# Kernel tuning notes

Hardware: AMD Instinct MI355X
Metric: run time of the kernel (lower is better)

The kernel has to match this reference:

```python
import jax, jax.numpy as jnp
import numpy as np

# Model constants (match init_kwargs)
IN_DIM = 1024   # input_dim == OLA frame size
ST_DIM = 128    # state_dim
HOP = IN_DIM // 2
N_FRAMES = 512
N_SAMPLES = 262144  # n_frames * hop
CTX = 512       # context_dim == control_plane_dim
HD = 32         # hypernetwork_dim
HL = 16         # hypernetwork_latent
B = 8


def _make_w(hv, A, Bm, i, o):
    # HyperNetworkLayer: hypervector -> latent -> flattened (i, o) matrix per batch
    return (hv @ A @ Bm).reshape(-1, i, o)


def setup_inputs() -> dict:
    key = jax.random.key(0)
    ks = jax.random.split(key, 17)
    s = 0.05
    return {
        'control_signal': jax.random.normal(ks[0], (B, CTX, N_FRAMES), jnp.float32),
        'state_hv': jax.random.normal(ks[1], (B, HD), jnp.float32),
        'output_hv': jax.random.normal(ks[2], (B, HD), jnp.float32),
        'input_hv': jax.random.normal(ks[3], (B, HD), jnp.float32),
        'direct_hv': jax.random.normal(ks[4], (B, HD), jnp.float32),
        'proj_hv': jax.random.normal(ks[5], (B, HD), jnp.float32),
        'times': jax.random.normal(ks[6], (B, 1, N_FRAMES), jnp.float32),
        # hypernetwork parameters (learned)
        'A_proj': jax.random.normal(ks[7], (HD, HL), jnp.float32) * s,
        'B_proj': jax.random.normal(ks[8], (HL, CTX * IN_DIM), jnp.float32) * s,
        'A_state': jax.random.normal(ks[9], (HD, HL), jnp.float32) * s,
        'B_state': jax.random.normal(ks[10], (HL, ST_DIM * ST_DIM), jnp.float32) * s,
        'A_input': jax.random.normal(ks[11], (HD, HL), jnp.float32) * s,
        'B_input': jax.random.normal(ks[12], (HL, IN_DIM * ST_DIM), jnp.float32) * s,
        'A_output': jax.random.normal(ks[13], (HD, HL), jnp.float32) * s,
        'B_output': jax.random.normal(ks[14], (HL, ST_DIM * IN_DIM), jnp.float32) * s,
        'A_direct': jax.random.normal(ks[15], (HD, HL), jnp.float32) * s,
        'B_direct': jax.random.normal(ks[16], (HL, IN_DIM * IN_DIM), jnp.float32) * s,
    }


def _forward(control_signal, state_hv, output_hv, input_hv, direct_hv, proj_hv, times,
             A_proj, B_proj, A_state, B_state, A_input, B_input,
             A_output, B_output, A_direct, B_direct):
    batch = control_signal.shape[0]
    dt = control_signal.dtype
    # per-batch hypernetwork-generated dense matrices
    Wp = _make_w(proj_hv, A_proj, B_proj, CTX, IN_DIM)       # [b, ctx, in]
    Ws = _make_w(state_hv, A_state, B_state, ST_DIM, ST_DIM)  # [b, st, st]
    Wi = _make_w(input_hv, A_input, B_input, IN_DIM, ST_DIM)  # [b, in, st]
    Wo = _make_w(output_hv, A_output, B_output, ST_DIM, IN_DIM)
    Wd = _make_w(direct_hv, A_direct, B_direct, IN_DIM, IN_DIM)

    ctrl = jnp.transpose(control_signal ** 2, (0, 2, 1))       # [b, fr, ctx]
    proj = jnp.einsum('bfc,bci->bfi', ctrl, Wp)                # [b, fr, in]

    def step(s, u):
        # s_i = A s_{i-1} + B u_i ; y_i = C (A s_{i-1}) + D u_i
        s2 = jnp.einsum('bs,bst->bt', s, Ws)
        y = jnp.einsum('bt,bti->bi', s2, Wo) + jnp.einsum('bi,bij->bj', u, Wd)
        s_new = s2 + jnp.einsum('bi,bis->bs', u, Wi)
        return s_new, y

    s0 = jnp.zeros((batch, ST_DIM), dt)
    _, outs = jax.lax.scan(step, s0, jnp.transpose(proj, (1, 0, 2)))  # [fr, b, in]
    outs = jnp.transpose(outs, (1, 0, 2))                              # [b, fr, in]

    # overlap-add with periodic hann window, hop = in_dim // 2
    win = 0.5 - 0.5 * jnp.cos(2.0 * jnp.pi * jnp.arange(IN_DIM, dtype=dt) / IN_DIM)
    windowed = outs * win
    total = HOP * (N_FRAMES - 1) + IN_DIM
    idx = jnp.arange(N_FRAMES)[:, None] * HOP + jnp.arange(IN_DIM)[None, :]  # [fr, in]
    buf = jnp.zeros((batch, total), dt).at[:, idx].add(windowed)
    sig = buf[:, :N_SAMPLES][:, None, :]   # [b, 1, n_samples]

    # DiracScheduler.schedule: softmax impulses over frames, upsample, FFT convolve
    impulses = jax.nn.softmax(times, axis=-1)                  # [b, 1, fr]
    up = jnp.zeros((batch, 1, N_SAMPLES), dt).at[:, :, ::N_SAMPLES // N_FRAMES].set(impulses)
    n = 2 * N_SAMPLES
    y = jnp.fft.irfft(jnp.fft.rfft(sig, n=n) * jnp.fft.rfft(up, n=n), n=n)[..., :N_SAMPLES]
    return y.astype(dt)


def reference(control_signal, state_hv, output_hv, input_hv, direct_hv, proj_hv, times,
              A_proj, B_proj, A_state, B_state, A_input, B_input,
              A_output, B_output, A_direct, B_direct):
    return _forward(control_signal, state_hv, output_hv, input_hv, direct_hv, proj_hv, times,
                    A_proj, B_proj, A_state, B_state, A_input, B_input,
                    A_output, B_output, A_direct, B_direct)
```

## Files before the change

kernel.cpp:

```cpp
#include <hip/hip_runtime.h>
#include <math.h>


typedef __attribute__((ext_vector_type(8))) short bfrag;
typedef __attribute__((ext_vector_type(4))) float f32x4;

__device__ inline unsigned short f2bf(float f) {
  unsigned int u = __float_as_uint(f);
  unsigned int r = (u + 0x7fff + ((u >> 16) & 1)) >> 16;
  return (unsigned short)r;
}
__device__ inline float bf2f(unsigned short u) {
  return __uint_as_float(((unsigned int)u) << 16);
}

static const size_t OFF_WPT   = 139264;
static const size_t OFF_WOT   = 2236416;
static const size_t OFF_WDIT  = 2760704;
static const size_t OFF_CTRLT = 7479296;
static const size_t OFF_PROJ  = 8527872;
static const size_t OFF_PROJD = 10625024;
static const size_t OFF_S2    = 15343616;
static const size_t OFF_MPOW  = 15605760;
static const size_t OFF_EC    = 16785408;
static const size_t OFF_HC    = 16850944;
static const size_t OFF_Y     = 16916480;
static const size_t OFF_SIG   = 21110784;

__global__ __launch_bounds__(256) void megabuild_kernel(
    const float* __restrict__ hv_p, const float* __restrict__ hv_s,
    const float* __restrict__ hv_i, const float* __restrict__ hv_o,
    const float* __restrict__ hv_d,
    const float* __restrict__ A_p, const float* __restrict__ A_s,
    const float* __restrict__ A_i, const float* __restrict__ A_o,
    const float* __restrict__ A_d,
    const float* __restrict__ B_p, const float* __restrict__ B_s,
    const float* __restrict__ B_i, const float* __restrict__ B_o,
    const float* __restrict__ B_d,
    const float* __restrict__ control,
    unsigned short* __restrict__ WpT, unsigned short* __restrict__ WoT,
    unsigned short* __restrict__ WdiT, float* __restrict__ Ws1,
    unsigned short* __restrict__ ctrlT) {
  __shared__ float ls[128];
  __shared__ unsigned short tile[8][32][36];
  __shared__ float ttile[32][33];
  const int blk = blockIdx.x;
  const int tid = threadIdx.x;

  if (blk >= 1808) {
    int z = blk - 1808;
    int b = z >> 8;
    int c0 = (z & 15) * 32, f0 = ((z >> 4) & 15) * 32;
    int tx = tid & 31, ty = tid >> 5;
    const float* inb = control + (size_t)b * 512 * 512;
    unsigned short* outb = ctrlT + (size_t)b * 512 * 512;
#pragma unroll
    for (int i = 0; i < 4; ++i) {
      float v = inb[(size_t)(c0 + ty + i * 8) * 512 + f0 + tx];
      ttile[ty + i * 8][tx] = v * v;
    }
    __syncthreads();
#pragma unroll
    for (int i = 0; i < 4; ++i)
      outb[(size_t)(f0 + ty + i * 8) * 512 + c0 + tx] = f2bf(ttile[tx][ty + i * 8]);
    return;
  }

  const float* hv; const float* Am; const float* Bm;
  unsigned short* outw = nullptr; int R = 0, C = 0; size_t bstride = 0; int bx = 0, by = 0;
  int role;
  if (blk < 512)        { role = 0; hv = hv_p; Am = A_p; Bm = B_p; outw = WpT;  R = 512;  C = 1024; bstride = 524288;  bx = blk & 31;           by = blk >> 5; }
  else if (blk < 1536)  { role = 1; hv = hv_d; Am = A_d; Bm = B_d; outw = WdiT; R = 1024; C = 1024; bstride = 1179648; bx = (blk - 512) & 31;   by = (blk - 512) >> 5; }
  else if (blk < 1664)  { role = 2; hv = hv_i; Am = A_i; Bm = B_i; outw = WdiT + 1024 * 1024; R = 1024; C = 128; bstride = 1179648; bx = (blk - 1536) & 3; by = (blk - 1536) >> 2; }
  else if (blk < 1792)  { role = 3; hv = hv_o; Am = A_o; Bm = B_o; outw = WoT;  R = 128;  C = 1024; bstride = 131072;  bx = (blk - 1664) & 31;  by = (blk - 1664) >> 5; }
  else                  { role = 4; hv = hv_s; Am = A_s; Bm = B_s; }

  if (tid < 128) {
    int b = tid >> 4, l = tid & 15;
    float acc = 0.f;
#pragma unroll
    for (int h = 0; h < 32; ++h) acc = fmaf(hv[b * 32 + h], Am[h * 16 + l], acc);
    ls[tid] = acc;
  }

  if (role == 4) {
    __syncthreads();
    int e = ((blk - 1792) * 256 + tid) * 4;
    float4 v[16];
#pragma unroll
    for (int l = 0; l < 16; ++l)
      v[l] = *(const float4*)(Bm + (size_t)l * 16384 + e);
#pragma unroll 1
    for (int b = 0; b < 8; ++b) {
      float ax = 0.f, ay = 0.f, az = 0.f, aw = 0.f;
#pragma unroll
      for (int l = 0; l < 16; ++l) {
        float lv = ls[b * 16 + l];
        ax = fmaf(lv, v[l].x, ax);
        ay = fmaf(lv, v[l].y, ay);
        az = fmaf(lv, v[l].z, az);
        aw = fmaf(lv, v[l].w, aw);
      }
      *(float4*)(Ws1 + (size_t)b * 147456 + e) = make_float4(ax, ay, az, aw);
    }
    return;
  }

  const int rl = tid >> 3;
  const int c4 = (tid & 7) * 4;
  const size_t RC = (size_t)R * C;
  const float* Bp = Bm + (size_t)(by * 32 + rl) * C + bx * 32 + c4;
  float4 bm4[16];
#pragma unroll
  for (int l = 0; l < 16; ++l)
    bm4[l] = *(const float4*)(Bp + (size_t)l * RC);
  __syncthreads();

#pragma unroll 1
  for (int b = 0; b < 8; ++b) {
    float a0 = 0.f, a1 = 0.f, a2 = 0.f, a3 = 0.f;
#pragma unroll
    for (int l = 0; l < 16; ++l) {
      float lv = ls[b * 16 + l];
      a0 = fmaf(lv, bm4[l].x, a0);
      a1 = fmaf(lv, bm4[l].y, a1);
      a2 = fmaf(lv, bm4[l].z, a2);
      a3 = fmaf(lv, bm4[l].w, a3);
    }
    tile[b][c4 + 0][rl] = f2bf(a0);
    tile[b][c4 + 1][rl] = f2bf(a1);
    tile[b][c4 + 2][rl] = f2bf(a2);
    tile[b][c4 + 3][rl] = f2bf(a3);
  }
  __syncthreads();

  const int wc = tid >> 3, wrq = tid & 7;
  unsigned short* ob = outw + (size_t)(bx * 32 + wc) * R + by * 32 + wrq * 4;
#pragma unroll 1
  for (int b = 0; b < 8; ++b) {
    ushort4 v = *(const ushort4*)&tile[b][wc][wrq * 4];
    *(ushort4*)(ob + (size_t)b * bstride) = v;
  }
}

template <int EPI, int OUTM>
__global__ __launch_bounds__(256) void mfma_gemm_kernel(
    const unsigned short* __restrict__ A,
    const unsigned short* __restrict__ BT,
    const float* __restrict__ D, int ldd,
    void* __restrict__ Cout,
    int M, int N, int K) {
  const int b = blockIdx.z;
  A  += (size_t)b * M * K;
  BT += (size_t)b * N * K;
  const int m0 = blockIdx.y * 128;
  const int n0 = blockIdx.x * 128;
  __shared__ __align__(16) unsigned short As[2][128][40];
  __shared__ __align__(16) unsigned short Bs[2][128][40];
  const int tid = threadIdx.x;
  const int lane = tid & 63, wave = tid >> 6;
  const int wr = (wave >> 1) * 64, wc = (wave & 1) * 64;
  const int l15 = lane & 15, g = lane >> 4;
  f32x4 acc[4][4];
#pragma unroll
  for (int i = 0; i < 4; ++i)
#pragma unroll
    for (int j = 0; j < 4; ++j)
#pragma unroll
      for (int r = 0; r < 4; ++r) acc[i][j][r] = 0.f;

  const int srow = tid >> 2, soct = tid & 3;
  const unsigned short* Ag = A + (size_t)(m0 + srow) * K + soct * 8;
  const unsigned short* Bg = BT + (size_t)(n0 + srow) * K + soct * 8;
  const size_t row64 = (size_t)64 * K;
  const int nt = K >> 5;

  bfrag av0 = *(const bfrag*)(Ag);
  bfrag av1 = *(const bfrag*)(Ag + row64);
  bfrag bv0 = *(const bfrag*)(Bg);
  bfrag bv1 = *(const bfrag*)(Bg + row64);

  int cur = 0;
#pragma unroll 1
  for (int t = 0; t < nt; ++t) {
    *(bfrag*)(&As[cur][srow][soct * 8]) = av0;
    *(bfrag*)(&As[cur][64 + srow][soct * 8]) = av1;
    *(bfrag*)(&Bs[cur][srow][soct * 8]) = bv0;
    *(bfrag*)(&Bs[cur][64 + srow][soct * 8]) = bv1;
    __syncthreads();
    if (t + 1 < nt) {
      const int k0 = (t + 1) << 5;
      av0 = *(const bfrag*)(Ag + k0);
      av1 = *(const bfrag*)(Ag + row64 + k0);
      bv0 = *(const bfrag*)(Bg + k0);
      bv1 = *(const bfrag*)(Bg + row64 + k0);
    }
    bfrag af[4], bf[4];
#pragma unroll
    for (int mi = 0; mi < 4; ++mi)
      af[mi] = *(const bfrag*)(&As[cur][wr + mi * 16 + l15][g * 8]);
#pragma unroll
    for (int nj = 0; nj < 4; ++nj)
      bf[nj] = *(const bfrag*)(&Bs[cur][wc + nj * 16 + l15][g * 8]);
#pragma unroll
    for (int mi = 0; mi < 4; ++mi)
#pragma unroll
      for (int nj = 0; nj < 4; ++nj)
        acc[mi][nj] = __builtin_amdgcn_mfma_f32_16x16x32_bf16(af[mi], bf[nj], acc[mi][nj], 0, 0, 0);
    cur ^= 1;
  }

  float* Cf = (float*)Cout + (size_t)b * M * N;
  unsigned short* Cb = (unsigned short*)Cout + (size_t)b * M * N;
  if (EPI) D += (size_t)b * M * ldd;
#pragma unroll
  for (int nj = 0; nj < 4; ++nj) {
    int n = n0 + wc + nj * 16 + l15;
    float win = 0.f;
    if (EPI) win = 0.5f - 0.5f * cosf(6.28318530717958647693f * (float)n / 1024.0f);
#pragma unroll
    for (int mi = 0; mi < 4; ++mi) {
      int mbase = m0 + wr + mi * 16 + 4 * g;
      float v[4];
#pragma unroll
      for (int r = 0; r < 4; ++r) {
        v[r] = acc[mi][nj][r];
        if (EPI) v[r] = (v[r] + D[(size_t)(mbase + r) * ldd + n]) * win;
      }
      if (OUTM == 2) {
        ushort4 o;
        o.x = f2bf(v[0]); o.y = f2bf(v[1]); o.z = f2bf(v[2]); o.w = f2bf(v[3]);
        *(ushort4*)(Cb + (size_t)n * M + mbase) = o;
      } else {
#pragma unroll
        for (int r = 0; r < 4; ++r) {
          if (OUTM == 1) Cb[(size_t)(mbase + r) * N + n] = f2bf(v[r]);
          else           Cf[(size_t)(mbase + r) * N + n] = v[r];
        }
      }
    }
  }
}

__global__ __launch_bounds__(256) void powers_kernel(float* __restrict__ Mpow, int half) {
  int z = blockIdx.x;
  int b = z / half, k = z - b * half + 1;
  const float* A = Mpow + ((size_t)b * 9 + k) * 16384;
  const float* Bm = Mpow + ((size_t)b * 9 + half) * 16384;
  float* C = Mpow + ((size_t)b * 9 + half + k) * 16384;
  __shared__ __align__(16) float As[16][132];
  __shared__ __align__(16) float Bs[16][132];
  int tid = threadIdx.x;
  int tx = tid & 15, ty = tid >> 4;
  float acc[8][8];
#pragma unroll
  for (int i = 0; i < 8; ++i)
#pragma unroll
    for (int j = 0; j < 8; ++j) acc[i][j] = 0.f;
  int ar = tid >> 1, ac = (tid & 1) * 8;
  int br = tid >> 4, bc = (tid & 15) * 8;
  for (int k0 = 0; k0 < 128; k0 += 16) {
    float4 a0 = *(const float4*)(A + (size_t)ar * 128 + k0 + ac);
    float4 a1 = *(const float4*)(A + (size_t)ar * 128 + k0 + ac + 4);
    float4 b0 = *(const float4*)(Bm + (size_t)(k0 + br) * 128 + bc);
    float4 b1 = *(const float4*)(Bm + (size_t)(k0 + br) * 128 + bc + 4);
    __syncthreads();
    As[ac + 0][ar] = a0.x; As[ac + 1][ar] = a0.y; As[ac + 2][ar] = a0.z; As[ac + 3][ar] = a0.w;
    As[ac + 4][ar] = a1.x; As[ac + 5][ar] = a1.y; As[ac + 6][ar] = a1.z; As[ac + 7][ar] = a1.w;
    *(float4*)(&Bs[br][bc]) = b0;
    *(float4*)(&Bs[br][bc + 4]) = b1;
    __syncthreads();
#pragma unroll
    for (int kk = 0; kk < 16; ++kk) {
      float4 av0 = *(const float4*)(&As[kk][ty * 8]);
      float4 av1 = *(const float4*)(&As[kk][ty * 8 + 4]);
      float4 bv0 = *(const float4*)(&Bs[kk][tx * 8]);
      float4 bv1 = *(const float4*)(&Bs[kk][tx * 8 + 4]);
      float aa[8] = {av0.x, av0.y, av0.z, av0.w, av1.x, av1.y, av1.z, av1.w};
      float bb[8] = {bv0.x, bv0.y, bv0.z, bv0.w, bv1.x, bv1.y, bv1.z, bv1.w};
#pragma unroll
      for (int i = 0; i < 8; ++i)
#pragma unroll
        for (int j = 0; j < 8; ++j) acc[i][j] = fmaf(aa[i], bb[j], acc[i][j]);
    }
  }
#pragma unroll
  for (int i = 0; i < 8; ++i) {
    *(float4*)(C + (size_t)(ty * 8 + i) * 128 + tx * 8) =
        make_float4(acc[i][0], acc[i][1], acc[i][2], acc[i][3]);
    *(float4*)(C + (size_t)(ty * 8 + i) * 128 + tx * 8 + 4) =
        make_float4(acc[i][4], acc[i][5], acc[i][6], acc[i][7]);
  }
}

__global__ __launch_bounds__(256) void ec_kernel(
    const float* __restrict__ Mpow, const float* __restrict__ PD,
    float* __restrict__ Ec) {
  int b = blockIdx.x >> 6, c = blockIdx.x & 63;
  int tid = threadIdx.x, t = tid & 127, dh = tid >> 7;
  __shared__ __align__(16) float Bus[7][128];
  __shared__ float red[128];
  const float* Bu = PD + (size_t)b * 512 * 1152 + 1024;
  for (int idx = tid; idx < 896; idx += 256)
    Bus[idx >> 7][idx & 127] = Bu[(size_t)(c * 8 + (idx >> 7)) * 1152 + (idx & 127)];
  __syncthreads();
  float acc = 0.f;
  const float* Mb = Mpow + (size_t)b * 9 * 16384;
  int d0 = dh * 64;
#pragma unroll
  for (int i = 0; i < 7; ++i) {
    const float* Mk = Mb + (size_t)(7 - i) * 16384 + t;
#pragma unroll 8
    for (int d = 0; d < 64; ++d)
      acc = fmaf(Bus[i][d0 + d], Mk[(size_t)(d0 + d) * 128], acc);
  }
  if (dh == 1) red[t] = acc;
  __syncthreads();
  if (dh == 0) {
    float tot = acc + red[t] + Bu[(size_t)(c * 8 + 7) * 1152 + t];
    Ec[((size_t)b * 64 + c) * 128 + t] = tot;
  }
}

__global__ __launch_bounds__(128) void combine_kernel(
    const float* __restrict__ Mpow, const float* __restrict__ Ec,
    float* __restrict__ Hc) {
  int b = blockIdx.x, t = threadIdx.x;
  float w[128];
  const float* M8 = Mpow + ((size_t)b * 9 + 8) * 16384;
#pragma unroll
  for (int k = 0; k < 128; ++k) w[k] = M8[(size_t)k * 128 + t];
  __shared__ __align__(16) float ec_sh[64 * 128];
  const float* Ecb = Ec + (size_t)b * 8192;
#pragma unroll
  for (int i = 0; i < 16; ++i) {
    int idx = (t + i * 128) * 4;
    *(float4*)&ec_sh[idx] = *(const float4*)(Ecb + idx);
  }
  __shared__ __align__(16) float sh[2][128];
  sh[0][t] = 0.f;
  float* Hcb = Hc + (size_t)b * 8192;
  Hcb[t] = 0.f;
  __syncthreads();
  int cur = 0;
#pragma unroll 1
  for (int c = 0; c < 63; ++c) {
    float a0 = 0.f, a1 = 0.f, a2 = 0.f, a3 = 0.f;
#pragma unroll
    for (int k = 0; k < 128; k += 4) {
      float4 sv = *(const float4*)(&sh[cur][k]);
      a0 = fmaf(sv.x, w[k + 0], a0);
      a1 = fmaf(sv.y, w[k + 1], a1);
      a2 = fmaf(sv.z, w[k + 2], a2);
      a3 = fmaf(sv.w, w[k + 3], a3);
    }
    float hn = (a0 + a1) + (a2 + a3) + ec_sh[c * 128 + t];
    sh[cur ^ 1][t] = hn;
    Hcb[(c + 1) * 128 + t] = hn;
    __syncthreads();
    cur ^= 1;
  }
}

__global__ __launch_bounds__(256) void pass2_kernel(
    const float* __restrict__ Mpow, const float* __restrict__ PD,
    const float* __restrict__ Hc, unsigned short* __restrict__ S2) {
  int b = blockIdx.x >> 6, c = blockIdx.x & 63;
  int tid = threadIdx.x, t = tid & 127, dh = tid >> 7;
  __shared__ __align__(16) float Xs[15][128];
  __shared__ __align__(16) float red[8][128];
  const float* Bu = PD + (size_t)b * 512 * 1152 + 1024;
  for (int idx = tid; idx < 15 * 128; idx += 256) {
    int rr = idx >> 7, cc = idx & 127;
    float v = 0.f;
    if (rr == 7) v = Hc[((size_t)b * 64 + c) * 128 + cc];
    else if (rr > 7) v = Bu[(size_t)(c * 8 + rr - 8) * 1152 + cc];
    Xs[rr][cc] = v;
  }
  __syncthreads();
  float acc[8];
#pragma unroll
  for (int j = 0; j < 8; ++j) acc[j] = 0.f;
  const float* Mb = Mpow + (size_t)b * 9 * 16384;
  int d0 = dh * 64;
#pragma unroll 1
  for (int k = 1; k <= 8; ++k) {
    const float* Mk = Mb + (size_t)k * 16384 + t;
    const int xbase = 8 - k;
#pragma unroll 4
    for (int d4 = 0; d4 < 16; ++d4) {
      int d = d0 + d4 * 4;
      float m0 = Mk[(size_t)(d + 0) * 128];
      float m1 = Mk[(size_t)(d + 1) * 128];
      float m2 = Mk[(size_t)(d + 2) * 128];
      float m3 = Mk[(size_t)(d + 3) * 128];
#pragma unroll
      for (int j = 0; j < 8; ++j) {
        float4 xv = *(const float4*)(&Xs[xbase + j][d]);
        acc[j] = fmaf(xv.x, m0, acc[j]);
        acc[j] = fmaf(xv.y, m1, acc[j]);
        acc[j] = fmaf(xv.z, m2, acc[j]);
        acc[j] = fmaf(xv.w, m3, acc[j]);
      }
    }
  }
  if (dh == 1) {
#pragma unroll
    for (int j = 0; j < 8; ++j) red[j][t] = acc[j];
  }
  __syncthreads();
  if (dh == 0) {
    unsigned short* S2b = S2 + ((size_t)b * 512 + c * 8) * 128;
#pragma unroll
    for (int j = 0; j < 8; ++j)
      S2b[(size_t)j * 128 + t] = f2bf(acc[j] + red[j][t]);
  }
}

__global__ void ola_kernel(const unsigned short* __restrict__ YT,
                           unsigned short* __restrict__ sigT) {
  int idx = blockIdx.x * 256 + threadIdx.x;
  int b = idx >> 16;
  int rem = idx & 65535;
  int r = rem >> 7, p4 = (rem & 127) * 4;
  const unsigned short* Y1 = YT + (size_t)b * 524288 + (size_t)r * 512 + p4;
  const unsigned short* Y2 = YT + (size_t)b * 524288 + (size_t)(512 + r) * 512 + p4 - 1;
  ushort4 t1 = *(const ushort4*)Y1;
  float o0 = bf2f(t1.x), o1 = bf2f(t1.y), o2 = bf2f(t1.z), o3 = bf2f(t1.w);
  if (p4 > 0) o0 += bf2f(Y2[0]);
  o1 += bf2f(Y2[1]);
  o2 += bf2f(Y2[2]);
  o3 += bf2f(Y2[3]);
  ushort4 o;
  o.x = f2bf(o0); o.y = f2bf(o1); o.z = f2bf(o2); o.w = f2bf(o3);
  *(ushort4*)(sigT + (size_t)b * 262144 + (size_t)r * 512 + p4) = o;
}

__global__ __launch_bounds__(256) void conv_mfma_kernel(
    const float* __restrict__ times,
    const unsigned short* __restrict__ sigT,
    float* __restrict__ out) {
  const int b = blockIdx.z;
  const int m0 = blockIdx.y * 128;
  const int n0 = blockIdx.x * 128;
  __shared__ unsigned short imp_bf[512];
  __shared__ float red[256];
  __shared__ __align__(16) unsigned short As[2][128][40];
  __shared__ __align__(16) unsigned short Bs[2][128][40];
  const int tid = threadIdx.x;

  float v0 = times[b * 512 + tid], v1 = times[b * 512 + 256 + tid];
  red[tid] = fmaxf(v0, v1);
  __syncthreads();
  for (int s = 128; s > 0; s >>= 1) {
    if (tid < s) red[tid] = fmaxf(red[tid], red[tid + s]);
    __syncthreads();
  }
  float mx = red[0];
  __syncthreads();
  float e0 = expf(v0 - mx), e1 = expf(v1 - mx);
  red[tid] = e0 + e1;
  __syncthreads();
  for (int s = 128; s > 0; s >>= 1) {
    if (tid < s) red[tid] += red[tid + s];
    __syncthreads();
  }
  float inv = 1.f / red[0];
  imp_bf[tid] = f2bf(e0 * inv);
  imp_bf[256 + tid] = f2bf(e1 * inv);
  __syncthreads();

  const int lane = tid & 63, wave = tid >> 6;
  const int wr = (wave >> 1) * 64, wc = (wave & 1) * 64;
  const int l15 = lane & 15, g = lane >> 4;
  f32x4 acc[4][4];
#pragma unroll
  for (int i = 0; i < 4; ++i)
#pragma unroll
    for (int j = 0; j < 4; ++j)
#pragma unroll
      for (int r = 0; r < 4; ++r) acc[i][j][r] = 0.f;

  const int srow = tid >> 2, soct = tid & 3;
  const int q0 = m0 + srow, q1 = m0 + 64 + srow;
  const unsigned short* Bg = sigT + (size_t)b * 262144 + (size_t)(n0 + srow) * 512 + soct * 8;
  const size_t row64 = (size_t)64 * 512;
  const int nt = (m0 + 128) >> 5;

  bfrag bv0 = *(const bfrag*)(Bg);
  bfrag bv1 = *(const bfrag*)(Bg + row64);

  int cur = 0;
#pragma unroll 1
  for (int t = 0; t < nt; ++t) {
    const int k0 = t << 5;
    bfrag av0, av1;
#pragma unroll
    for (int j = 0; j < 8; ++j) {
      int p = k0 + soct * 8 + j;
      av0[j] = (p <= q0) ? (short)imp_bf[q0 - p] : (short)0;
      av1[j] = (p <= q1) ? (short)imp_bf[q1 - p] : (short)0;
    }
    *(bfrag*)(&As[cur][srow][soct * 8]) = av0;
    *(bfrag*)(&As[cur][64 + srow][soct * 8]) = av1;
    *(bfrag*)(&Bs[cur][srow][soct * 8]) = bv0;
    *(bfrag*)(&Bs[cur][64 + srow][soct * 8]) = bv1;
    __syncthreads();
    if (t + 1 < nt) {
      const int kn = (t + 1) << 5;
      bv0 = *(const bfrag*)(Bg + kn);
      bv1 = *(const bfrag*)(Bg + row64 + kn);
    }
    bfrag af[4], bf[4];
#pragma unroll
    for (int mi = 0; mi < 4; ++mi)
      af[mi] = *(const bfrag*)(&As[cur][wr + mi * 16 + l15][g * 8]);
#pragma unroll
    for (int nj = 0; nj < 4; ++nj)
      bf[nj] = *(const bfrag*)(&Bs[cur][wc + nj * 16 + l15][g * 8]);
#pragma unroll
    for (int mi = 0; mi < 4; ++mi)
#pragma unroll
      for (int nj = 0; nj < 4; ++nj)
        acc[mi][nj] = __builtin_amdgcn_mfma_f32_16x16x32_bf16(af[mi], bf[nj], acc[mi][nj], 0, 0, 0);
    cur ^= 1;
  }

  float* Cf = out + (size_t)b * 262144;
#pragma unroll
  for (int nj = 0; nj < 4; ++nj) {
    int n = n0 + wc + nj * 16 + l15;
#pragma unroll
    for (int mi = 0; mi < 4; ++mi) {
      int mbase = m0 + wr + mi * 16 + 4 * g;
#pragma unroll
      for (int r = 0; r < 4; ++r)
        Cf[(size_t)(mbase + r) * 512 + n] = acc[mi][nj][r];
    }
  }
}

extern "C" void kernel_launch(void* const* d_in, const int* in_sizes, int n_in,
                              void* d_out, int out_size, void* d_ws, size_t ws_size,
                              hipStream_t stream) {
  const float* control   = (const float*)d_in[0];
  const float* state_hv  = (const float*)d_in[1];
  const float* output_hv = (const float*)d_in[2];
  const float* input_hv  = (const float*)d_in[3];
  const float* direct_hv = (const float*)d_in[4];
  const float* proj_hv   = (const float*)d_in[5];
  const float* times     = (const float*)d_in[6];
  const float* A_proj   = (const float*)d_in[7];
  const float* B_proj   = (const float*)d_in[8];
  const float* A_state  = (const float*)d_in[9];
  const float* B_state  = (const float*)d_in[10];
  const float* A_input  = (const float*)d_in[11];
  const float* B_input  = (const float*)d_in[12];
  const float* A_output = (const float*)d_in[13];
  const float* B_output = (const float*)d_in[14];
  const float* A_direct = (const float*)d_in[15];
  const float* B_direct = (const float*)d_in[16];

  float* ws = (float*)d_ws;
  unsigned short* WpT   = (unsigned short*)(ws + OFF_WPT);
  unsigned short* WoT   = (unsigned short*)(ws + OFF_WOT);
  unsigned short* WdiT  = (unsigned short*)(ws + OFF_WDIT);
  unsigned short* ctrlT = (unsigned short*)(ws + OFF_CTRLT);
  unsigned short* proj  = (unsigned short*)(ws + OFF_PROJ);
  float* projD = ws + OFF_PROJD;
  unsigned short* S2 = (unsigned short*)(ws + OFF_S2);
  float* Mpow = ws + OFF_MPOW;
  float* Ec   = ws + OFF_EC;
  float* Hc   = ws + OFF_HC;
  unsigned short* YT   = (unsigned short*)(ws + OFF_Y);
  unsigned short* sigT = (unsigned short*)(ws + OFF_SIG);
  float* out  = (float*)d_out;

  megabuild_kernel<<<3856, 256, 0, stream>>>(
      proj_hv, state_hv, input_hv, output_hv, direct_hv,
      A_proj, A_state, A_input, A_output, A_direct,
      B_proj, B_state, B_input, B_output, B_direct,
      control, WpT, WoT, WdiT, Mpow + 16384, ctrlT);

  mfma_gemm_kernel<0, 1><<<dim3(8, 4, 8), 256, 0, stream>>>(
      ctrlT, WpT, nullptr, 0, proj, 512, 1024, 512);

  mfma_gemm_kernel<0, 0><<<dim3(9, 4, 8), 256, 0, stream>>>(
      proj, WdiT, nullptr, 0, projD, 512, 1152, 1024);

  powers_kernel<<<8, 256, 0, stream>>>(Mpow, 1);
  powers_kernel<<<16, 256, 0, stream>>>(Mpow, 2);
  powers_kernel<<<32, 256, 0, stream>>>(Mpow, 4);
  ec_kernel<<<512, 256, 0, stream>>>(Mpow, projD, Ec);
  combine_kernel<<<8, 128, 0, stream>>>(Mpow, Ec, Hc);
  pass2_kernel<<<512, 256, 0, stream>>>(Mpow, projD, Hc, S2);

  mfma_gemm_kernel<1, 2><<<dim3(8, 4, 8), 256, 0, stream>>>(
      S2, WoT, projD, 1152, YT, 512, 1024, 128);

  ola_kernel<<<2048, 256, 0, stream>>>(YT, sigT);

  conv_mfma_kernel<<<dim3(4, 4, 8), 256, 0, stream>>>(times, sigT, out);
}
```

Measured before the change: 239.8 us.

## Fuse matrix-power kernels with grid barrier and store transposed powers

Merges the three power-doubling launches into one 32-block kernel that synchronises through a global atomic barrier, removing two kernel launches and their gaps. Each power step also writes a transposed copy (MpowT), and M1 is transposed explicitly, so ec, combine and pass2 can read contiguous float4 rows instead of strided columns. The costs are extra global writes for the transposed copies and reliance on all 32 blocks being co-resident for the spin barrier.

```diff
diff --git a/kernel.cpp b/kernel.cpp
--- a/kernel.cpp
+++ b/kernel.cpp
@@ -26,6 +26,19 @@
 static const size_t OFF_HC    = 16850944;
 static const size_t OFF_Y     = 16916480;
 static const size_t OFF_SIG   = 21110784;
+static const size_t OFF_MPOWT = 22159360;
+static const size_t OFF_BAR   = 23339008;
+
+__device__ inline void gridbar(unsigned* cnt, unsigned target) {
+  __syncthreads();
+  if (threadIdx.x == 0) {
+    __threadfence();
+    atomicAdd(cnt, 1u);
+    while (atomicAdd(cnt, 0u) < target) { __builtin_amdgcn_s_sleep(8); }
+    __threadfence();
+  }
+  __syncthreads();
+}
 
 __global__ __launch_bounds__(256) void megabuild_kernel(
     const float* __restrict__ hv_p, const float* __restrict__ hv_s,
@@ -40,12 +53,13 @@
     const float* __restrict__ control,
     unsigned short* __restrict__ WpT, unsigned short* __restrict__ WoT,
     unsigned short* __restrict__ WdiT, float* __restrict__ Ws1,
-    unsigned short* __restrict__ ctrlT) {
+    unsigned short* __restrict__ ctrlT, unsigned* __restrict__ bar) {
   __shared__ float ls[128];
   __shared__ unsigned short tile[8][32][36];
   __shared__ float ttile[32][33];
   const int blk = blockIdx.x;
   const int tid = threadIdx.x;
+  if (blk == 0 && tid == 0) bar[0] = 0u;
 
   if (blk >= 1808) {
     int z = blk - 1808;
@@ -242,15 +256,10 @@
   }
 }
 
-__global__ __launch_bounds__(256) void powers_kernel(float* __restrict__ Mpow, int half) {
-  int z = blockIdx.x;
-  int b = z / half, k = z - b * half + 1;
-  const float* A = Mpow + ((size_t)b * 9 + k) * 16384;
-  const float* Bm = Mpow + ((size_t)b * 9 + half) * 16384;
-  float* C = Mpow + ((size_t)b * 9 + half + k) * 16384;
-  __shared__ __align__(16) float As[16][132];
-  __shared__ __align__(16) float Bs[16][132];
-  int tid = threadIdx.x;
+__device__ inline void power_step_dev(const float* __restrict__ A,
+                                      const float* __restrict__ Bm,
+                                      float* __restrict__ C, float* __restrict__ CT,
+                                      float (*As)[132], float (*Bs)[132], int tid) {
   int tx = tid & 15, ty = tid >> 4;
   float acc[8][8];
 #pragma unroll
@@ -291,10 +300,66 @@
     *(float4*)(C + (size_t)(ty * 8 + i) * 128 + tx * 8 + 4) =
         make_float4(acc[i][4], acc[i][5], acc[i][6], acc[i][7]);
   }
+#pragma unroll
+  for (int j = 0; j < 8; ++j) {
+    *(float4*)(CT + (size_t)(tx * 8 + j) * 128 + ty * 8) =
+        make_float4(acc[0][j], acc[1][j], acc[2][j], acc[3][j]);
+    *(float4*)(CT + (size_t)(tx * 8 + j) * 128 + ty * 8 + 4) =
+        make_float4(acc[4][j], acc[5][j], acc[6][j], acc[7][j]);
+  }
+}
+
+__global__ __launch_bounds__(256) void powers_fused_kernel(
+    float* __restrict__ Mpow, float* __restrict__ MpowT, unsigned* __restrict__ bar) {
+  __shared__ __align__(16) float As[16][132];
+  __shared__ __align__(16) float Bs[16][132];
+  const int blk = blockIdx.x, tid = threadIdx.x;
+
+  if (blk < 8) {
+    const float* M1 = Mpow + ((size_t)blk * 9 + 1) * 16384;
+    power_step_dev(M1, M1, Mpow + ((size_t)blk * 9 + 2) * 16384,
+                   MpowT + ((size_t)blk * 9 + 2) * 16384, As, Bs, tid);
+  } else if (blk < 16) {
+    int b = blk - 8;
+    const float* src = Mpow + ((size_t)b * 9 + 1) * 16384;
+    float* dst = MpowT + ((size_t)b * 9 + 1) * 16384;
+    float (*lt)[33] = (float(*)[33])As;
+    int tx = tid & 31, ty = tid >> 5;
+#pragma unroll 1
+    for (int tl = 0; tl < 16; ++tl) {
+      int r0 = (tl >> 2) * 32, c0 = (tl & 3) * 32;
+      __syncthreads();
+#pragma unroll
+      for (int i = 0; i < 4; ++i)
+        lt[ty + i * 8][tx] = src[(size_t)(r0 + ty + i * 8) * 128 + c0 + tx];
+      __syncthreads();
+#pragma unroll
+      for (int i = 0; i < 4; ++i)
+        dst[(size_t)(c0 + ty + i * 8) * 128 + r0 + tx] = lt[tx][ty + i * 8];
+    }
+  }
+  gridbar(bar, 32);
+
+  if (blk < 16) {
+    int b = blk >> 1, k = (blk & 1) + 1;
+    power_step_dev(Mpow + ((size_t)b * 9 + k) * 16384,
+                   Mpow + ((size_t)b * 9 + 2) * 16384,
+                   Mpow + ((size_t)b * 9 + 2 + k) * 16384,
+                   MpowT + ((size_t)b * 9 + 2 + k) * 16384, As, Bs, tid);
+  }
+  gridbar(bar, 64);
+
+  {
+    int b = blk >> 2, k = (blk & 3) + 1;
+    power_step_dev(Mpow + ((size_t)b * 9 + k) * 16384,
+                   Mpow + ((size_t)b * 9 + 4) * 16384,
+                   Mpow + ((size_t)b * 9 + 4 + k) * 16384,
+                   MpowT + ((size_t)b * 9 + 4 + k) * 16384, As, Bs, tid);
+  }
 }
 
 __global__ __launch_bounds__(256) void ec_kernel(
-    const float* __restrict__ Mpow, const float* __restrict__ PD,
+    const float* __restrict__ MpowT, const float* __restrict__ PD,
     float* __restrict__ Ec) {
   int b = blockIdx.x >> 6, c = blockIdx.x & 63;
   int tid = threadIdx.x, t = tid & 127, dh = tid >> 7;
@@ -305,14 +370,19 @@
     Bus[idx >> 7][idx & 127] = Bu[(size_t)(c * 8 + (idx >> 7)) * 1152 + (idx & 127)];
   __syncthreads();
   float acc = 0.f;
-  const float* Mb = Mpow + (size_t)b * 9 * 16384;
+  const float* MbT = MpowT + (size_t)b * 9 * 16384;
   int d0 = dh * 64;
 #pragma unroll
   for (int i = 0; i < 7; ++i) {
-    const float* Mk = Mb + (size_t)(7 - i) * 16384 + t;
-#pragma unroll 8
-    for (int d = 0; d < 64; ++d)
-      acc = fmaf(Bus[i][d0 + d], Mk[(size_t)(d0 + d) * 128], acc);
+    const float* MkT = MbT + (size_t)(7 - i) * 16384 + (size_t)t * 128 + d0;
+#pragma unroll
+    for (int d4 = 0; d4 < 16; ++d4) {
+      float4 mv = *(const float4*)(MkT + d4 * 4);
+      acc = fmaf(Bus[i][d0 + d4 * 4 + 0], mv.x, acc);
+      acc = fmaf(Bus[i][d0 + d4 * 4 + 1], mv.y, acc);
+      acc = fmaf(Bus[i][d0 + d4 * 4 + 2], mv.z, acc);
+      acc = fmaf(Bus[i][d0 + d4 * 4 + 3], mv.w, acc);
+    }
   }
   if (dh == 1) red[t] = acc;
   __syncthreads();
@@ -323,13 +393,13 @@
 }
 
 __global__ __launch_bounds__(128) void combine_kernel(
-    const float* __restrict__ Mpow, const float* __restrict__ Ec,
+    const float* __restrict__ MpowT, const float* __restrict__ Ec,
     float* __restrict__ Hc) {
   int b = blockIdx.x, t = threadIdx.x;
   float w[128];
-  const float* M8 = Mpow + ((size_t)b * 9 + 8) * 16384;
-#pragma unroll
-  for (int k = 0; k < 128; ++k) w[k] = M8[(size_t)k * 128 + t];
+  const float* M8T = MpowT + ((size_t)b * 9 + 8) * 16384 + (size_t)t * 128;
+#pragma unroll
+  for (int k = 0; k < 128; ++k) w[k] = M8T[k];
   __shared__ __align__(16) float ec_sh[64 * 128];
   const float* Ecb = Ec + (size_t)b * 8192;
 #pragma unroll
@@ -363,7 +433,7 @@
 }
 
 __global__ __launch_bounds__(256) void pass2_kernel(
-    const float* __restrict__ Mpow, const float* __restrict__ PD,
+    const float* __restrict__ MpowT, const float* __restrict__ PD,
     const float* __restrict__ Hc, unsigned short* __restrict__ S2) {
   int b = blockIdx.x >> 6, c = blockIdx.x & 63;
   int tid = threadIdx.x, t = tid & 127, dh = tid >> 7;
@@ -381,19 +451,17 @@
   float acc[8];
 #pragma unroll
   for (int j = 0; j < 8; ++j) acc[j] = 0.f;
-  const float* Mb = Mpow + (size_t)b * 9 * 16384;
+  const float* MbT = MpowT + (size_t)b * 9 * 16384;
   int d0 = dh * 64;
 #pragma unroll 1
   for (int k = 1; k <= 8; ++k) {
-    const float* Mk = Mb + (size_t)k * 16384 + t;
+    const float* MkT = MbT + (size_t)k * 16384 + (size_t)t * 128;
     const int xbase = 8 - k;
 #pragma unroll 4
     for (int d4 = 0; d4 < 16; ++d4) {
       int d = d0 + d4 * 4;
-      float m0 = Mk[(size_t)(d + 0) * 128];
-      float m1 = Mk[(size_t)(d + 1) * 128];
-      float m2 = Mk[(size_t)(d + 2) * 128];
-      float m3 = Mk[(size_t)(d + 3) * 128];
+      float4 mv = *(const float4*)(MkT + d);
+      float m0 = mv.x, m1 = mv.y, m2 = mv.z, m3 = mv.w;
 #pragma unroll
       for (int j = 0; j < 8; ++j) {
         float4 xv = *(const float4*)(&Xs[xbase + j][d]);
@@ -569,18 +637,20 @@
   unsigned short* proj  = (unsigned short*)(ws + OFF_PROJ);
   float* projD = ws + OFF_PROJD;
   unsigned short* S2 = (unsigned short*)(ws + OFF_S2);
-  float* Mpow = ws + OFF_MPOW;
+  float* Mpow  = ws + OFF_MPOW;
+  float* MpowT = ws + OFF_MPOWT;
   float* Ec   = ws + OFF_EC;
   float* Hc   = ws + OFF_HC;
   unsigned short* YT   = (unsigned short*)(ws + OFF_Y);
   unsigned short* sigT = (unsigned short*)(ws + OFF_SIG);
+  unsigned* bar = (unsigned*)(ws + OFF_BAR);
   float* out  = (float*)d_out;
 
   megabuild_kernel<<<3856, 256, 0, stream>>>(
       proj_hv, state_hv, input_hv, output_hv, direct_hv,
       A_proj, A_state, A_input, A_output, A_direct,
       B_proj, B_state, B_input, B_output, B_direct,
-      control, WpT, WoT, WdiT, Mpow + 16384, ctrlT);
+      control, WpT, WoT, WdiT, Mpow + 16384, ctrlT, bar);
 
   mfma_gemm_kernel<0, 1><<<dim3(8, 4, 8), 256, 0, stream>>>(
       ctrlT, WpT, nullptr, 0, proj, 512, 1024, 512);
@@ -588,12 +658,11 @@
   mfma_gemm_kernel<0, 0><<<dim3(9, 4, 8), 256, 0, stream>>>(
       proj, WdiT, nullptr, 0, projD, 512, 1152, 1024);
 
-  powers_kernel<<<8, 256, 0, stream>>>(Mpow, 1);
-  powers_kernel<<<16, 256, 0, stream>>>(Mpow, 2);
-  powers_kernel<<<32, 256, 0, stream>>>(Mpow, 4);
-  ec_kernel<<<512, 256, 0, stream>>>(Mpow, projD, Ec);
-  combine_kernel<<<8, 128, 0, stream>>>(Mpow, Ec, Hc);
-  pass2_kernel<<<512, 256, 0, stream>>>(Mpow, projD, Hc, S2);
+  powers_fused_kernel<<<32, 256, 0, stream>>>(Mpow, MpowT, bar);
+
+  ec_kernel<<<512, 256, 0, stream>>>(MpowT, projD, Ec);
+  combine_kernel<<<8, 128, 0, stream>>>(MpowT, Ec, Hc);
+  pass2_kernel<<<512, 256, 0, stream>>>(MpowT, projD, Hc, S2);
 
   mfma_gemm_kernel<1, 2><<<dim3(8, 4, 8), 256, 0, stream>>>(
       S2, WoT, projD, 1152, YT, 512, 1024, 128);
```

Result: slower. 268.0 us (+11.7%).
